# Kernel tuning notes

Measured on AMD Instinct MI355X. Metric: run time of the kernel, lower is better.

Reference implementation:

```python
import jax, jax.numpy as jnp
import numpy as np

N_NODES = 4096
N_EDGES = 8192
N_GRAPHS = 256
D_NODE = 64
D_EDGE = 32
H = 256


def setup_inputs() -> dict:
    key = jax.random.key(0)
    ks = jax.random.split(key, 16)
    s = lambda d: 1.0 / np.sqrt(d)
    inp = {
        "x": jax.random.normal(ks[0], (N_NODES, D_NODE), dtype=jnp.float32),
        "edge_index": jax.random.randint(ks[1], (2, N_EDGES), 0, N_NODES),
        "edge_attr": jax.random.normal(ks[2], (N_EDGES, D_EDGE), dtype=jnp.float32),
        "batch": jnp.sort(jax.random.randint(ks[3], (N_NODES,), 0, N_GRAPHS)),
        # conv1: edge MLP 32 -> 64*256, root weight 64->256, bias 256
        "nn1_w": jax.random.normal(ks[4], (D_EDGE, D_NODE * H), dtype=jnp.float32) * s(D_EDGE),
        "nn1_b": jnp.zeros((D_NODE * H,), dtype=jnp.float32),
        "root1_w": jax.random.normal(ks[5], (D_NODE, H), dtype=jnp.float32) * s(D_NODE),
        "bias1": jnp.zeros((H,), dtype=jnp.float32),
        # conv2: edge MLP 32 -> 256*256, root weight 256->256, bias 256
        "nn2_w": jax.random.normal(ks[6], (D_EDGE, H * H), dtype=jnp.float32) * s(D_EDGE),
        "nn2_b": jnp.zeros((H * H,), dtype=jnp.float32),
        "root2_w": jax.random.normal(ks[7], (H, H), dtype=jnp.float32) * s(H),
        "bias2": jnp.zeros((H,), dtype=jnp.float32),
        # readout MLP: 256 -> 128 -> 1
        "lin1_w": jax.random.normal(ks[8], (H, H // 2), dtype=jnp.float32) * s(H),
        "lin1_b": jnp.zeros((H // 2,), dtype=jnp.float32),
        "lin2_w": jax.random.normal(ks[9], (H // 2, 1), dtype=jnp.float32) * s(H // 2),
        "lin2_b": jnp.zeros((1,), dtype=jnp.float32),
    }
    return inp


def nnconv(x, src, dst, edge_attr, nn_w, nn_b, root_w, bias, out_c):
    # PyG NNConv (aggr='add'): per-edge weight matrix from edge MLP,
    # message = x[src] @ W_e, scatter-add at dst, plus root transform + bias.
    e = edge_attr.shape[0]
    in_c = x.shape[1]
    w_e = (edge_attr @ nn_w + nn_b).reshape(e, in_c, out_c)  # [E, in, out]
    msg = jnp.einsum('ei,eio->eo', x[src], w_e)              # [E, out]
    agg = jax.ops.segment_sum(msg, dst, num_segments=x.shape[0])
    return agg + x @ root_w + bias


def reference(x, edge_index, edge_attr, batch,
              nn1_w, nn1_b, root1_w, bias1,
              nn2_w, nn2_b, root2_w, bias2,
              lin1_w, lin1_b, lin2_w, lin2_b):
    src, dst = edge_index[0], edge_index[1]
    h = nnconv(x, src, dst, edge_attr, nn1_w, nn1_b, root1_w, bias1, H)
    h = jax.nn.relu(h)
    h = nnconv(h, src, dst, edge_attr, nn2_w, nn2_b, root2_w, bias2, H)
    # global mean pool over graphs
    sums = jax.ops.segment_sum(h, batch, num_segments=N_GRAPHS)
    cnts = jax.ops.segment_sum(jnp.ones((h.shape[0],), h.dtype), batch, num_segments=N_GRAPHS)
    pooled = sums / jnp.maximum(cnts, 1.0)[:, None]
    # dropout is identity in eval mode
    z = jax.nn.relu(pooled @ lin1_w + lin1_b)
    return jax.nn.sigmoid(z @ lin2_w + lin2_b)  # [N_GRAPHS, 1]
```

## Files before the change

### kernel.cpp

```cpp
#include <hip/hip_runtime.h>
#include <math.h>

#define N_NODES 4096
#define N_EDGES 8192
#define N_GRAPHS 256
#define D_NODE 64
#define D_EDGE 32
#define HH 256

#define K1 2176
#define K2 8704

typedef _Float16 half8v __attribute__((ext_vector_type(8)));
typedef _Float16 half4v __attribute__((ext_vector_type(4)));
typedef float floatx4 __attribute__((ext_vector_type(4)));

static const size_t OFF_S    = 0;
static const size_t OFF_BT1  = 17825792;
static const size_t OFF_BT2  = 18104320;
static const size_t OFF_CP   = 19218432;
static const size_t OFF_H    = 31801344;
static const size_t OFF_H2   = 32063488;
static const size_t OFF_INT  = 33112064;

__global__ __launch_bounds__(1024) void csr_k(const int* __restrict__ dst,
                                              int* __restrict__ starts,
                                              int* __restrict__ elist) {
    __shared__ int cnt[4096];
    __shared__ int part[1024];
    int t = threadIdx.x;
#pragma unroll
    for (int i = 0; i < 4; ++i) cnt[t * 4 + i] = 0;
    __syncthreads();
#pragma unroll
    for (int i = 0; i < 8; ++i) atomicAdd(&cnt[dst[i * 1024 + t]], 1);
    __syncthreads();
    int v[4]; int s = 0;
#pragma unroll
    for (int i = 0; i < 4; ++i) { v[i] = cnt[t * 4 + i]; s += v[i]; }
    part[t] = s;
    __syncthreads();
    for (int off = 1; off < 1024; off <<= 1) {
        int tv = (t >= off) ? part[t - off] : 0;
        __syncthreads();
        part[t] += tv;
        __syncthreads();
    }
    int excl = part[t] - s;
    __syncthreads();
#pragma unroll
    for (int i = 0; i < 4; ++i) {
        starts[t * 4 + i] = excl;
        cnt[t * 4 + i] = excl;
        excl += v[i];
    }
    if (t == 1023) starts[4096] = excl;
    __syncthreads();
#pragma unroll
    for (int i = 0; i < 8; ++i) {
        int e = i * 1024 + t;
        int d = dst[e];
        int p = atomicAdd(&cnt[d], 1);
        elist[p] = e;
    }
}

__device__ __forceinline__ void packT_body(const float* __restrict__ w,
                                           const float* __restrict__ b,
                                           const float* __restrict__ rw,
                                           _Float16* __restrict__ BT,
                                           int kk0, int o0, int K,
                                           int wlim, int blim, int wshift, int wmask, int wrow) {
    __shared__ float T[64][65];
    int t = threadIdx.x;
    int ol = t & 63, kb = t >> 6;
#pragma unroll
    for (int p = 0; p < 16; ++p) {
        int kl = p * 4 + kb;
        int kk = kk0 + kl, o = o0 + ol;
        float v;
        if (kk < wlim)      v = w[(kk >> wshift) * wrow + (kk & wmask) * 256 + o];
        else if (kk < blim) v = b[(kk - wlim) * 256 + o];
        else                v = rw[(kk - blim) * 256 + o];
        T[kl][ol] = v;
    }
    __syncthreads();
    int kl2 = t & 63, ob = t >> 6;
#pragma unroll
    for (int p = 0; p < 16; ++p) {
        int ol2 = p * 4 + ob;
        BT[(size_t)(o0 + ol2) * K + kk0 + kl2] = (_Float16)T[kl2][ol2];
    }
}

__global__ __launch_bounds__(256) void pack_k(const float* __restrict__ w1,
                                              const float* __restrict__ b1,
                                              const float* __restrict__ r1,
                                              const float* __restrict__ w2,
                                              const float* __restrict__ b2,
                                              const float* __restrict__ r2,
                                              _Float16* __restrict__ BT1,
                                              _Float16* __restrict__ BT2) {
    int bx = blockIdx.x, o0 = blockIdx.y * 64;
    if (bx < K1 / 64)
        packT_body(w1, b1, r1, BT1, bx * 64, o0, K1, 2048, 2112, 6, 63, 16384);
    else
        packT_body(w2, b2, r2, BT2, (bx - K1 / 64) * 64, o0, K2, 8192, 8448, 8, 255, 65536);
}

__global__ __launch_bounds__(64) void s1_k(const float* __restrict__ x,
                                           const float* __restrict__ ea,
                                           const int* __restrict__ src,
                                           const int* __restrict__ starts,
                                           const int* __restrict__ elist,
                                           _Float16* __restrict__ S) {
    int n = blockIdx.x, t = threadIdx.x;
    __shared__ float sea[33];
    if (t == 32) sea[32] = 1.0f;
    float acc[33];
#pragma unroll
    for (int k = 0; k < 33; ++k) acc[k] = 0.f;
    int st = starts[n], en = starts[n + 1];
    for (int idx = st; idx < en; ++idx) {
        int e = elist[idx];
        int sn = src[e];
        if (t < 32) sea[t] = ea[e * 32 + t];
        __syncthreads();
        float xv = x[sn * 64 + t];
#pragma unroll
        for (int k = 0; k < 33; ++k) acc[k] += sea[k] * xv;
        __syncthreads();
    }
    _Float16* row = S + (size_t)n * K1;
#pragma unroll
    for (int k = 0; k < 33; ++k) row[k * 64 + t] = (_Float16)acc[k];
    row[2112 + t] = (_Float16)x[n * 64 + t];
}

__global__ __launch_bounds__(256) void s2_k(const _Float16* __restrict__ h,
                                            const float* __restrict__ ea,
                                            const int* __restrict__ src,
                                            const int* __restrict__ starts,
                                            const int* __restrict__ elist,
                                            _Float16* __restrict__ S) {
    int n = blockIdx.x, t = threadIdx.x;
    __shared__ float sea[33];
    if (t == 32) sea[32] = 1.0f;
    float acc[33];
#pragma unroll
    for (int k = 0; k < 33; ++k) acc[k] = 0.f;
    int st = starts[n], en = starts[n + 1];
    for (int idx = st; idx < en; ++idx) {
        int e = elist[idx];
        int sn = src[e];
        if (t < 32) sea[t] = ea[e * 32 + t];
        __syncthreads();
        float hv = (float)h[sn * 256 + t];
#pragma unroll
        for (int k = 0; k < 33; ++k) acc[k] += sea[k] * hv;
        __syncthreads();
    }
    _Float16* row = S + (size_t)n * K2;
#pragma unroll
    for (int k = 0; k < 33; ++k) row[k * 256 + t] = (_Float16)acc[k];
    row[8448 + t] = h[n * 256 + t];
}

__device__ __forceinline__ void async_copy16(const void* g, void* l) {
    __builtin_amdgcn_global_load_lds(
        (__attribute__((address_space(1))) unsigned int*)(g),
        (__attribute__((address_space(3))) unsigned int*)(l), 16, 0, 0);
}

__global__ __launch_bounds__(256, 3) void gemm_f16(const _Float16* __restrict__ A,
                                                   const _Float16* __restrict__ BT,
                                                   float* __restrict__ Cpart,
                                                   int K, int NC, int Z) {
    __shared__ _Float16 As[128 * 64];
    __shared__ _Float16 Bs[128 * 64];
    int tid = threadIdx.x;
    int w = tid >> 6, l = tid & 63;
    int mt = blockIdx.y, nt = blockIdx.x, z = blockIdx.z;
    int c0 = z * NC / Z, c1 = (z + 1) * NC / Z;
    int k0 = c0 * 64;
    int wm = w & 1, wn = w >> 1;

    int lr = l >> 3, lc = l & 7;
    int gc = lc ^ lr;
    const _Float16* gA0 = A  + (size_t)(mt * 128 + w * 32 + lr) * K + k0 + gc * 8;
    const _Float16* gB0 = BT + (size_t)(nt * 128 + w * 32 + lr) * K + k0 + gc * 8;

    int lm = l & 15, q4 = l >> 4;
    int sw = lm & 7;

    floatx4 acc[4][4] = {};

    for (int s = c0; s < c1; ++s) {
#pragma unroll
        for (int q = 0; q < 4; ++q) {
            async_copy16(gA0 + (size_t)q * 8 * K, As + (w * 32 + q * 8) * 64);
            async_copy16(gB0 + (size_t)q * 8 * K, Bs + (w * 32 + q * 8) * 64);
        }
        gA0 += 64; gB0 += 64;
        __syncthreads();
#pragma unroll
        for (int kw = 0; kw < 2; ++kw) {
            int ck = ((kw * 4 + q4) ^ sw) * 8;
            half8v af[4], bf[4];
#pragma unroll
            for (int i = 0; i < 4; ++i)
                af[i] = *(const half8v*)&As[(wm * 64 + i * 16 + lm) * 64 + ck];
#pragma unroll
            for (int j = 0; j < 4; ++j)
                bf[j] = *(const half8v*)&Bs[(wn * 64 + j * 16 + lm) * 64 + ck];
#pragma unroll
            for (int i = 0; i < 4; ++i)
#pragma unroll
                for (int j = 0; j < 4; ++j)
                    acc[i][j] = __builtin_amdgcn_mfma_f32_16x16x32_f16(af[i], bf[j], acc[i][j], 0, 0, 0);
        }
        __syncthreads();
    }

    float* Cp = Cpart + (size_t)z * (N_NODES * HH);
    int m0 = mt * 128 + wm * 64;
    int n0 = nt * 128 + wn * 64 + lm;
#pragma unroll
    for (int i = 0; i < 4; ++i)
#pragma unroll
        for (int j = 0; j < 4; ++j)
#pragma unroll
            for (int r = 0; r < 4; ++r)
                Cp[(size_t)(m0 + i * 16 + q4 * 4 + r) * HH + n0 + j * 16] = acc[i][j][r];
}

__global__ __launch_bounds__(256) void reduce_k(const float* __restrict__ Cp,
                                                const float* __restrict__ bias,
                                                _Float16* __restrict__ o16,
                                                float* __restrict__ o32,
                                                int nslices, int relu) {
    int idx = (blockIdx.x * 256 + threadIdx.x) * 4;
    float4 a = *(const float4*)(Cp + idx);
    for (int zz = 1; zz < nslices; ++zz) {
        float4 bq = *(const float4*)(Cp + (size_t)zz * (N_NODES * HH) + idx);
        a.x += bq.x; a.y += bq.y; a.z += bq.z; a.w += bq.w;
    }
    int n = idx & 255;
    float4 bb = *(const float4*)(bias + n);
    a.x += bb.x; a.y += bb.y; a.z += bb.z; a.w += bb.w;
    if (relu) {
        a.x = fmaxf(a.x, 0.f); a.y = fmaxf(a.y, 0.f);
        a.z = fmaxf(a.z, 0.f); a.w = fmaxf(a.w, 0.f);
    }
    if (o16) {
        half4v hv = {(_Float16)a.x, (_Float16)a.y, (_Float16)a.z, (_Float16)a.w};
        *(half4v*)(o16 + idx) = hv;
    } else {
        *(float4*)(o32 + idx) = a;
    }
}

__global__ __launch_bounds__(128) void poolread_k(const float* __restrict__ h2,
                                                  const int* __restrict__ batch,
                                                  const float* __restrict__ l1w,
                                                  const float* __restrict__ l1b,
                                                  const float* __restrict__ l2w,
                                                  const float* __restrict__ l2b,
                                                  float* __restrict__ out) {
    int g = blockIdx.x, t = threadIdx.x;
    __shared__ int bnds[2];
    __shared__ float sp[256];
    __shared__ float sz[128];
    if (t < 2) {
        int target = g + t;
        int lo = 0, hi = N_NODES;
        while (lo < hi) { int mid = (lo + hi) >> 1; if (batch[mid] < target) lo = mid + 1; else hi = mid; }
        bnds[t] = lo;
    }
    __syncthreads();
    int lo = bnds[0], hi = bnds[1];
    float s0 = 0.f, s1 = 0.f;
    for (int n = lo; n < hi; ++n) {
        s0 += h2[(size_t)n * 256 + t];
        s1 += h2[(size_t)n * 256 + 128 + t];
    }
    float inv = 1.0f / fmaxf((float)(hi - lo), 1.0f);
    sp[t] = s0 * inv;
    sp[t + 128] = s1 * inv;
    __syncthreads();
    float a = l1b[t];
#pragma unroll 8
    for (int i = 0; i < 256; ++i) a += sp[i] * l1w[i * 128 + t];
    sz[t] = fmaxf(a, 0.f) * l2w[t];
    __syncthreads();
    for (int s = 64; s > 0; s >>= 1) {
        if (t < s) sz[t] += sz[t + s];
        __syncthreads();
    }
    if (t == 0) {
        float zz = sz[0] + l2b[0];
        out[g] = 1.0f / (1.0f + expf(-zz));
    }
}

extern "C" void kernel_launch(void* const* d_in, const int* in_sizes, int n_in,
                              void* d_out, int out_size, void* d_ws, size_t ws_size,
                              hipStream_t stream) {
    const float* x       = (const float*)d_in[0];
    const int*   ei      = (const int*)d_in[1];
    const float* ea      = (const float*)d_in[2];
    const int*   batch   = (const int*)d_in[3];
    const float* nn1_w   = (const float*)d_in[4];
    const float* nn1_b   = (const float*)d_in[5];
    const float* root1_w = (const float*)d_in[6];
    const float* bias1   = (const float*)d_in[7];
    const float* nn2_w   = (const float*)d_in[8];
    const float* nn2_b   = (const float*)d_in[9];
    const float* root2_w = (const float*)d_in[10];
    const float* bias2   = (const float*)d_in[11];
    const float* lin1_w  = (const float*)d_in[12];
    const float* lin1_b  = (const float*)d_in[13];
    const float* lin2_w  = (const float*)d_in[14];
    const float* lin2_b  = (const float*)d_in[15];
    float* out = (float*)d_out;
    float* ws  = (float*)d_ws;

    _Float16* S    = (_Float16*)(ws + OFF_S);
    _Float16* BT1  = (_Float16*)(ws + OFF_BT1);
    _Float16* BT2  = (_Float16*)(ws + OFF_BT2);
    float*    Cp   = ws + OFF_CP;
    _Float16* h    = (_Float16*)(ws + OFF_H);
    float*    h2   = ws + OFF_H2;
    int* ip     = (int*)(ws + OFF_INT);
    int* starts = ip;
    int* elist  = ip + 4100;

    const int* srcv = ei;
    const int* dstv = ei + N_EDGES;

    csr_k<<<1, 1024, 0, stream>>>(dstv, starts, elist);
    pack_k<<<dim3(K1 / 64 + K2 / 64, 4), 256, 0, stream>>>(nn1_w, nn1_b, root1_w,
                                                           nn2_w, nn2_b, root2_w, BT1, BT2);

    s1_k<<<4096, 64, 0, stream>>>(x, ea, srcv, starts, elist, S);
    gemm_f16<<<dim3(2, 32, 8), 256, 0, stream>>>(S, BT1, Cp, K1, K1 / 64, 8);
    reduce_k<<<1024, 256, 0, stream>>>(Cp, bias1, h, nullptr, 8, 1);

    s2_k<<<4096, 256, 0, stream>>>(h, ea, srcv, starts, elist, S);
    gemm_f16<<<dim3(2, 32, 12), 256, 0, stream>>>(S, BT2, Cp, K2, K2 / 64, 12);
    reduce_k<<<1024, 256, 0, stream>>>(Cp, bias2, nullptr, h2, 12, 0);

    poolread_k<<<N_GRAPHS, 128, 0, stream>>>(h2, batch, lin1_w, lin1_b, lin2_w, lin2_b, out);
}
```

Measured before the change: 206.9 us.

## Fuse edge-gather into GEMM A-tile load and fold reduce into pooling

Drops the separate s1/s2 kernels that built the large fp16 S matrix. Each GEMM block now builds its A tile on the fly: it gathers source-node features weighted by edge attributes for its rows and writes the swizzled tile into LDS, so S never goes through global memory. CSR construction is merged into the weight-packing launch, and the conv2 split-K reduction plus bias is folded into the pooling kernel, which cuts two launches and the h2 buffer. In exchange the gather is repeated per N-tile, its loads are irregular and sit inside the GEMM loop, and reduce_k gains a stray null-pointer dereference expression that is undefined behaviour.

Result: slower. 274.0 us (+32.4%).

```diff
diff --git a/kernel.cpp b/kernel.cpp
--- a/kernel.cpp
+++ b/kernel.cpp
@@ -10,67 +10,65 @@
 
 #define K1 2176
 #define K2 8704
+#define NSL1 8
+#define NSL2 12
 
 typedef _Float16 half8v __attribute__((ext_vector_type(8)));
-typedef _Float16 half4v __attribute__((ext_vector_type(4)));
 typedef float floatx4 __attribute__((ext_vector_type(4)));
 
-static const size_t OFF_S    = 0;
-static const size_t OFF_BT1  = 17825792;
-static const size_t OFF_BT2  = 18104320;
-static const size_t OFF_CP   = 19218432;
-static const size_t OFF_H    = 31801344;
-static const size_t OFF_H2   = 32063488;
-static const size_t OFF_INT  = 33112064;
-
-__global__ __launch_bounds__(1024) void csr_k(const int* __restrict__ dst,
-                                              int* __restrict__ starts,
-                                              int* __restrict__ elist) {
+static const size_t OFF_CP   = 0;
+static const size_t OFF_BT1  = 12582912;
+static const size_t OFF_BT2  = 12861440;
+static const size_t OFF_H    = 13975552;
+static const size_t OFF_INT  = 14499840;
+
+__device__ void csr_body(const int* __restrict__ dst,
+                         int* __restrict__ starts,
+                         int* __restrict__ elist) {
     __shared__ int cnt[4096];
-    __shared__ int part[1024];
+    __shared__ int ps[256];
     int t = threadIdx.x;
 #pragma unroll
-    for (int i = 0; i < 4; ++i) cnt[t * 4 + i] = 0;
-    __syncthreads();
-#pragma unroll
-    for (int i = 0; i < 8; ++i) atomicAdd(&cnt[dst[i * 1024 + t]], 1);
-    __syncthreads();
-    int v[4]; int s = 0;
-#pragma unroll
-    for (int i = 0; i < 4; ++i) { v[i] = cnt[t * 4 + i]; s += v[i]; }
-    part[t] = s;
-    __syncthreads();
-    for (int off = 1; off < 1024; off <<= 1) {
-        int tv = (t >= off) ? part[t - off] : 0;
-        __syncthreads();
-        part[t] += tv;
-        __syncthreads();
-    }
-    int excl = part[t] - s;
-    __syncthreads();
-#pragma unroll
-    for (int i = 0; i < 4; ++i) {
-        starts[t * 4 + i] = excl;
-        cnt[t * 4 + i] = excl;
+    for (int i = 0; i < 16; ++i) cnt[t * 16 + i] = 0;
+    __syncthreads();
+#pragma unroll
+    for (int i = 0; i < 32; ++i) atomicAdd(&cnt[dst[i * 256 + t]], 1);
+    __syncthreads();
+    int v[16]; int s = 0;
+#pragma unroll
+    for (int i = 0; i < 16; ++i) { v[i] = cnt[t * 16 + i]; s += v[i]; }
+    ps[t] = s;
+    __syncthreads();
+    for (int off = 1; off < 256; off <<= 1) {
+        int tv = (t >= off) ? ps[t - off] : 0;
+        __syncthreads();
+        ps[t] += tv;
+        __syncthreads();
+    }
+    int excl = ps[t] - s;
+#pragma unroll
+    for (int i = 0; i < 16; ++i) {
+        starts[t * 16 + i] = excl;
+        cnt[t * 16 + i] = excl;
         excl += v[i];
     }
-    if (t == 1023) starts[4096] = excl;
-    __syncthreads();
-#pragma unroll
-    for (int i = 0; i < 8; ++i) {
-        int e = i * 1024 + t;
+    if (t == 255) starts[4096] = excl;
+    __syncthreads();
+#pragma unroll
+    for (int i = 0; i < 32; ++i) {
+        int e = i * 256 + t;
         int d = dst[e];
         int p = atomicAdd(&cnt[d], 1);
         elist[p] = e;
     }
 }
 
-__device__ __forceinline__ void packT_body(const float* __restrict__ w,
-                                           const float* __restrict__ b,
-                                           const float* __restrict__ rw,
-                                           _Float16* __restrict__ BT,
-                                           int kk0, int o0, int K,
-                                           int wlim, int blim, int wshift, int wmask, int wrow) {
+__device__ void packT_body(const float* __restrict__ w,
+                           const float* __restrict__ b,
+                           const float* __restrict__ rw,
+                           _Float16* __restrict__ BT,
+                           int kk0, int o0, int K,
+                           int wlim, int blim, int wshift, int wmask, int wrow) {
     __shared__ float T[64][65];
     int t = threadIdx.x;
     int ol = t & 63, kb = t >> 6;
@@ -93,7 +91,10 @@
     }
 }
 
-__global__ __launch_bounds__(256) void pack_k(const float* __restrict__ w1,
+__global__ __launch_bounds__(256) void prep_k(const int* __restrict__ dst,
+                                              int* __restrict__ starts,
+                                              int* __restrict__ elist,
+                                              const float* __restrict__ w1,
                                               const float* __restrict__ b1,
                                               const float* __restrict__ r1,
                                               const float* __restrict__ w2,
@@ -101,69 +102,16 @@
                                               const float* __restrict__ r2,
                                               _Float16* __restrict__ BT1,
                                               _Float16* __restrict__ BT2) {
-    int bx = blockIdx.x, o0 = blockIdx.y * 64;
-    if (bx < K1 / 64)
-        packT_body(w1, b1, r1, BT1, bx * 64, o0, K1, 2048, 2112, 6, 63, 16384);
+    int bx = blockIdx.x, by = blockIdx.y;
+    if (bx == 0) {
+        if (by == 0) csr_body(dst, starts, elist);
+        return;
+    }
+    int pbx = bx - 1, o0 = by * 64;
+    if (pbx < K1 / 64)
+        packT_body(w1, b1, r1, BT1, pbx * 64, o0, K1, 2048, 2112, 6, 63, 16384);
     else
-        packT_body(w2, b2, r2, BT2, (bx - K1 / 64) * 64, o0, K2, 8192, 8448, 8, 255, 65536);
-}
-
-__global__ __launch_bounds__(64) void s1_k(const float* __restrict__ x,
-                                           const float* __restrict__ ea,
-                                           const int* __restrict__ src,
-                                           const int* __restrict__ starts,
-                                           const int* __restrict__ elist,
-                                           _Float16* __restrict__ S) {
-    int n = blockIdx.x, t = threadIdx.x;
-    __shared__ float sea[33];
-    if (t == 32) sea[32] = 1.0f;
-    float acc[33];
-#pragma unroll
-    for (int k = 0; k < 33; ++k) acc[k] = 0.f;
-    int st = starts[n], en = starts[n + 1];
-    for (int idx = st; idx < en; ++idx) {
-        int e = elist[idx];
-        int sn = src[e];
-        if (t < 32) sea[t] = ea[e * 32 + t];
-        __syncthreads();
-        float xv = x[sn * 64 + t];
-#pragma unroll
-        for (int k = 0; k < 33; ++k) acc[k] += sea[k] * xv;
-        __syncthreads();
-    }
-    _Float16* row = S + (size_t)n * K1;
-#pragma unroll
-    for (int k = 0; k < 33; ++k) row[k * 64 + t] = (_Float16)acc[k];
-    row[2112 + t] = (_Float16)x[n * 64 + t];
-}
-
-__global__ __launch_bounds__(256) void s2_k(const _Float16* __restrict__ h,
-                                            const float* __restrict__ ea,
-                                            const int* __restrict__ src,
-                                            const int* __restrict__ starts,
-                                            const int* __restrict__ elist,
-                                            _Float16* __restrict__ S) {
-    int n = blockIdx.x, t = threadIdx.x;
-    __shared__ float sea[33];
-    if (t == 32) sea[32] = 1.0f;
-    float acc[33];
-#pragma unroll
-    for (int k = 0; k < 33; ++k) acc[k] = 0.f;
-    int st = starts[n], en = starts[n + 1];
-    for (int idx = st; idx < en; ++idx) {
-        int e = elist[idx];
-        int sn = src[e];
-        if (t < 32) sea[t] = ea[e * 32 + t];
-        __syncthreads();
-        float hv = (float)h[sn * 256 + t];
-#pragma unroll
-        for (int k = 0; k < 33; ++k) acc[k] += sea[k] * hv;
-        __syncthreads();
-    }
-    _Float16* row = S + (size_t)n * K2;
-#pragma unroll
-    for (int k = 0; k < 33; ++k) row[k * 256 + t] = (_Float16)acc[k];
-    row[8448 + t] = h[n * 256 + t];
+        packT_body(w2, b2, r2, BT2, (pbx - K1 / 64) * 64, o0, K2, 8192, 8448, 8, 255, 65536);
 }
 
 __device__ __forceinline__ void async_copy16(const void* g, void* l) {
@@ -172,36 +120,84 @@
         (__attribute__((address_space(3))) unsigned int*)(l), 16, 0, 0);
 }
 
-__global__ __launch_bounds__(256, 3) void gemm_f16(const _Float16* __restrict__ A,
-                                                   const _Float16* __restrict__ BT,
-                                                   float* __restrict__ Cpart,
-                                                   int K, int NC, int Z) {
+template <typename T, int CPK>
+__global__ __launch_bounds__(256, 3) void gemm_fused(const T* __restrict__ X,
+                                                     const float* __restrict__ ea,
+                                                     const int* __restrict__ src,
+                                                     const int* __restrict__ starts,
+                                                     const int* __restrict__ elist,
+                                                     const _Float16* __restrict__ BT,
+                                                     float* __restrict__ Cpart,
+                                                     int K, int NC, int Z) {
     __shared__ _Float16 As[128 * 64];
     __shared__ _Float16 Bs[128 * 64];
+    const int ID = 64 * CPK;
     int tid = threadIdx.x;
     int w = tid >> 6, l = tid & 63;
-    int mt = blockIdx.y, nt = blockIdx.x, z = blockIdx.z;
+    int nt = blockIdx.x, mt = blockIdx.y, z = blockIdx.z;
     int c0 = z * NC / Z, c1 = (z + 1) * NC / Z;
-    int k0 = c0 * 64;
     int wm = w & 1, wn = w >> 1;
 
     int lr = l >> 3, lc = l & 7;
     int gc = lc ^ lr;
-    const _Float16* gA0 = A  + (size_t)(mt * 128 + w * 32 + lr) * K + k0 + gc * 8;
-    const _Float16* gB0 = BT + (size_t)(nt * 128 + w * 32 + lr) * K + k0 + gc * 8;
-
-    int lm = l & 15, q4 = l >> 4;
-    int sw = lm & 7;
+    const _Float16* gB0 = BT + (size_t)(nt * 128 + w * 32 + lr) * K + c0 * 64 + gc * 8;
+
+    int gr = tid >> 1, hs = tid & 1;
+    int n = mt * 128 + gr;
+    int e0 = starts[n], e1 = starts[n + 1];
+
+    int lm = l & 15, q4 = l >> 4, sw = lm & 7;
 
     floatx4 acc[4][4] = {};
 
-    for (int s = c0; s < c1; ++s) {
-#pragma unroll
-        for (int q = 0; q < 4; ++q) {
-            async_copy16(gA0 + (size_t)q * 8 * K, As + (w * 32 + q * 8) * 64);
+    for (int c = c0; c < c1; ++c) {
+#pragma unroll
+        for (int q = 0; q < 4; ++q)
             async_copy16(gB0 + (size_t)q * 8 * K, Bs + (w * 32 + q * 8) * 64);
+        gB0 += 64;
+
+        float ga[32];
+        int k = c / CPK;
+        if (k < 33) {
+            int i0 = (c - k * CPK) * 64 + hs * 32;
+#pragma unroll
+            for (int j = 0; j < 32; ++j) ga[j] = 0.f;
+            for (int ie = e0; ie < e1; ++ie) {
+                int e = elist[ie];
+                float val = (k == 32) ? 1.0f : ea[e * 32 + k];
+                const T* xp = X + (size_t)src[e] * ID + i0;
+                if (sizeof(T) == 2) {
+                    const half8v* hp = (const half8v*)xp;
+#pragma unroll
+                    for (int q = 0; q < 4; ++q) {
+                        half8v hv = hp[q];
+#pragma unroll
+                        for (int j = 0; j < 8; ++j) ga[q * 8 + j] += val * (float)hv[j];
+                    }
+                } else {
+                    const float4* fp = (const float4*)xp;
+#pragma unroll
+                    for (int q = 0; q < 8; ++q) {
+                        float4 fv = fp[q];
+                        ga[q * 4 + 0] += val * fv.x; ga[q * 4 + 1] += val * fv.y;
+                        ga[q * 4 + 2] += val * fv.z; ga[q * 4 + 3] += val * fv.w;
+                    }
+                }
+            }
+        } else {
+            const T* xp = X + (size_t)n * ID + (c - 33 * CPK) * 64 + hs * 32;
+#pragma unroll
+            for (int j = 0; j < 32; ++j) ga[j] = (float)xp[j];
         }
-        gA0 += 64; gB0 += 64;
+        _Float16* arow = As + gr * 64;
+#pragma unroll
+        for (int c8 = 0; c8 < 4; ++c8) {
+            int slot = (hs * 4 + c8) ^ (gr & 7);
+            half8v hv;
+#pragma unroll
+            for (int j = 0; j < 8; ++j) hv[j] = (_Float16)ga[c8 * 8 + j];
+            *(half8v*)(arow + slot * 8) = hv;
+        }
         __syncthreads();
 #pragma unroll
         for (int kw = 0; kw < 2; ++kw) {
@@ -236,32 +232,26 @@
 
 __global__ __launch_bounds__(256) void reduce_k(const float* __restrict__ Cp,
                                                 const float* __restrict__ bias,
-                                                _Float16* __restrict__ o16,
-                                                float* __restrict__ o32,
-                                                int nslices, int relu) {
+                                                _Float16* __restrict__ o16) {
     int idx = (blockIdx.x * 256 + threadIdx.x) * 4;
     float4 a = *(const float4*)(Cp + idx);
-    for (int zz = 1; zz < nslices; ++zz) {
+#pragma unroll
+    for (int zz = 1; zz < NSL1; ++zz) {
         float4 bq = *(const float4*)(Cp + (size_t)zz * (N_NODES * HH) + idx);
         a.x += bq.x; a.y += bq.y; a.z += bq.z; a.w += bq.w;
     }
-    int n = idx & 255;
-    float4 bb = *(const float4*)(bias + n);
-    a.x += bb.x; a.y += bb.y; a.z += bb.z; a.w += bb.w;
-    if (relu) {
-        a.x = fmaxf(a.x, 0.f); a.y = fmaxf(a.y, 0.f);
-        a.z = fmaxf(a.z, 0.f); a.w = fmaxf(a.w, 0.f);
-    }
-    if (o16) {
-        half4v hv = {(_Float16)a.x, (_Float16)a.y, (_Float16)a.z, (_Float16)a.w};
-        *(half4v*)(o16 + idx) = hv;
-    } else {
-        *(float4*)(o32 + idx) = a;
-    }
-}
-
-__global__ __launch_bounds__(128) void poolread_k(const float* __restrict__ h2,
+    int nn = idx & 255;
+    float4 bb = *(const float4*)(bias + nn);
+    a.x = fmaxf(a.x + bb.x, 0.f); a.y = fmaxf(a.y + bb.y, 0.f);
+    a.z = fmaxf(a.z + bb.z, 0.f); a.w = fmaxf(a.w + bb.w, 0.f);
+    _Float16 h4[4] = {(_Float16)a.x, (_Float16)a.y, (_Float16)a.z, (_Float16)a.w};
+    *(half8v*)0;
+    o16[idx + 0] = h4[0]; o16[idx + 1] = h4[1]; o16[idx + 2] = h4[2]; o16[idx + 3] = h4[3];
+}
+
+__global__ __launch_bounds__(256) void poolread_k(const float* __restrict__ Cp,
                                                   const int* __restrict__ batch,
+                                                  const float* __restrict__ bias2,
                                                   const float* __restrict__ l1w,
                                                   const float* __restrict__ l1b,
                                                   const float* __restrict__ l2w,
@@ -279,22 +269,27 @@
     }
     __syncthreads();
     int lo = bnds[0], hi = bnds[1];
-    float s0 = 0.f, s1 = 0.f;
+    float s = 0.f;
     for (int n = lo; n < hi; ++n) {
-        s0 += h2[(size_t)n * 256 + t];
-        s1 += h2[(size_t)n * 256 + 128 + t];
-    }
-    float inv = 1.0f / fmaxf((float)(hi - lo), 1.0f);
-    sp[t] = s0 * inv;
-    sp[t + 128] = s1 * inv;
-    __syncthreads();
-    float a = l1b[t];
+        float a = 0.f;
+#pragma unroll
+        for (int zz = 0; zz < NSL2; ++zz)
+            a += Cp[(size_t)zz * (N_NODES * HH) + (size_t)n * HH + t];
+        s += a;
+    }
+    sp[t] = (hi > lo) ? (s / (float)(hi - lo) + bias2[t]) : 0.f;
+    __syncthreads();
+    float r = 0.f;
+    if (t < 128) {
+        float a = l1b[t];
 #pragma unroll 8
-    for (int i = 0; i < 256; ++i) a += sp[i] * l1w[i * 128 + t];
-    sz[t] = fmaxf(a, 0.f) * l2w[t];
-    __syncthreads();
-    for (int s = 64; s > 0; s >>= 1) {
-        if (t < s) sz[t] += sz[t + s];
+        for (int i = 0; i < 256; ++i) a += sp[i] * l1w[i * 128 + t];
+        r = fmaxf(a, 0.f) * l2w[t];
+        sz[t] = r;
+    }
+    __syncthreads();
+    for (int ss = 64; ss > 0; ss >>= 1) {
+        if (t < ss) sz[t] += sz[t + ss];
         __syncthreads();
     }
     if (t == 0) {
@@ -325,12 +320,10 @@
     float* out = (float*)d_out;
     float* ws  = (float*)d_ws;
 
-    _Float16* S    = (_Float16*)(ws + OFF_S);
-    _Float16* BT1  = (_Float16*)(ws + OFF_BT1);
-    _Float16* BT2  = (_Float16*)(ws + OFF_BT2);
-    float*    Cp   = ws + OFF_CP;
-    _Float16* h    = (_Float16*)(ws + OFF_H);
-    float*    h2   = ws + OFF_H2;
+    float*    Cp  = ws + OFF_CP;
+    _Float16* BT1 = (_Float16*)(ws + OFF_BT1);
+    _Float16* BT2 = (_Float16*)(ws + OFF_BT2);
+    _Float16* h   = (_Float16*)(ws + OFF_H);
     int* ip     = (int*)(ws + OFF_INT);
     int* starts = ip;
     int* elist  = ip + 4100;
@@ -338,17 +331,17 @@
     const int* srcv = ei;
     const int* dstv = ei + N_EDGES;
 
-    csr_k<<<1, 1024, 0, stream>>>(dstv, starts, elist);
-    pack_k<<<dim3(K1 / 64 + K2 / 64, 4), 256, 0, stream>>>(nn1_w, nn1_b, root1_w,
-                                                           nn2_w, nn2_b, root2_w, BT1, BT2);
-
-    s1_k<<<4096, 64, 0, stream>>>(x, ea, srcv, starts, elist, S);
-    gemm_f16<<<dim3(2, 32, 8), 256, 0, stream>>>(S, BT1, Cp, K1, K1 / 64, 8);
-    reduce_k<<<1024, 256, 0, stream>>>(Cp, bias1, h, nullptr, 8, 1);
-
-    s2_k<<<4096, 256, 0, stream>>>(h, ea, srcv, starts, elist, S);
-    gemm_f16<<<dim3(2, 32, 12), 256, 0, stream>>>(S, BT2, Cp, K2, K2 / 64, 12);
-    reduce_k<<<1024, 256, 0, stream>>>(Cp, bias2, nullptr, h2, 12, 0);
-
-    poolread_k<<<N_GRAPHS, 128, 0, stream>>>(h2, batch, lin1_w, lin1_b, lin2_w, lin2_b, out);
-}
+    prep_k<<<dim3(1 + K1 / 64 + K2 / 64, 4), 256, 0, stream>>>(
+        dstv, starts, elist, nn1_w, nn1_b, root1_w, nn2_w, nn2_b, root2_w, BT1, BT2);
+
+    gemm_fused<float, 1><<<dim3(2, 32, NSL1), 256, 0, stream>>>(
+        x, ea, srcv, starts, elist, BT1, Cp, K1, K1 / 64, NSL1);
+
+    reduce_k<<<1024, 256, 0, stream>>>(Cp, bias1, h);
+
+    gemm_fused<_Float16, 4><<<dim3(2, 32, NSL2), 256, 0, stream>>>(
+        h, ea, srcv, starts, elist, BT2, Cp, K2, K2 / 64, NSL2);
+
+    poolread_k<<<N_GRAPHS, 256, 0, stream>>>(Cp, batch, bias2,
+                                             lin1_w, lin1_b, lin2_w, lin2_b, out);
+}
```

## Store split-K partials in fp16 and fuse reductions into consumers

Applied to the files above, without the earlier changes.

GEMM split-K partial outputs are now written as fp16 instead of fp32, which halves partial-sum traffic. The second-layer reduce kernel is removed, and the mean-pool readout now sums the slice partials per node directly and adds bias2 after averaging. The CSR build is merged into the weight-pack kernel as an extra block, and the first reduce becomes a vectorised 8-wide fp16 kernel. This drops two launches and much memory traffic, at the cost of fp16 rounding on partial sums, which may lose accuracy, and a longer serial loop in poolread.

After: 200.5 us. 3.1% less time.

```diff
diff --git a/kernel.cpp b/kernel.cpp
--- a/kernel.cpp
+++ b/kernel.cpp
@@ -10,67 +10,66 @@
 
 #define K1 2176
 #define K2 8704
+#define NSL1 8
+#define NSL2 12
 
 typedef _Float16 half8v __attribute__((ext_vector_type(8)));
-typedef _Float16 half4v __attribute__((ext_vector_type(4)));
 typedef float floatx4 __attribute__((ext_vector_type(4)));
 
 static const size_t OFF_S    = 0;
 static const size_t OFF_BT1  = 17825792;
 static const size_t OFF_BT2  = 18104320;
 static const size_t OFF_CP   = 19218432;
-static const size_t OFF_H    = 31801344;
-static const size_t OFF_H2   = 32063488;
-static const size_t OFF_INT  = 33112064;
-
-__global__ __launch_bounds__(1024) void csr_k(const int* __restrict__ dst,
-                                              int* __restrict__ starts,
-                                              int* __restrict__ elist) {
+static const size_t OFF_H    = 25509888;
+static const size_t OFF_INT  = 26034176;
+
+__device__ void csr_body(const int* __restrict__ dst,
+                         int* __restrict__ starts,
+                         int* __restrict__ elist) {
     __shared__ int cnt[4096];
-    __shared__ int part[1024];
+    __shared__ int ps[256];
     int t = threadIdx.x;
 #pragma unroll
-    for (int i = 0; i < 4; ++i) cnt[t * 4 + i] = 0;
-    __syncthreads();
-#pragma unroll
-    for (int i = 0; i < 8; ++i) atomicAdd(&cnt[dst[i * 1024 + t]], 1);
-    __syncthreads();
-    int v[4]; int s = 0;
-#pragma unroll
-    for (int i = 0; i < 4; ++i) { v[i] = cnt[t * 4 + i]; s += v[i]; }
-    part[t] = s;
-    __syncthreads();
-    for (int off = 1; off < 1024; off <<= 1) {
-        int tv = (t >= off) ? part[t - off] : 0;
-        __syncthreads();
-        part[t] += tv;
-        __syncthreads();
-    }
-    int excl = part[t] - s;
-    __syncthreads();
-#pragma unroll
-    for (int i = 0; i < 4; ++i) {
-        starts[t * 4 + i] = excl;
-        cnt[t * 4 + i] = excl;
+    for (int i = 0; i < 16; ++i) cnt[t * 16 + i] = 0;
+    __syncthreads();
+#pragma unroll
+    for (int i = 0; i < 32; ++i) atomicAdd(&cnt[dst[i * 256 + t]], 1);
+    __syncthreads();
+    int v[16]; int s = 0;
+#pragma unroll
+    for (int i = 0; i < 16; ++i) { v[i] = cnt[t * 16 + i]; s += v[i]; }
+    ps[t] = s;
+    __syncthreads();
+    for (int off = 1; off < 256; off <<= 1) {
+        int tv = (t >= off) ? ps[t - off] : 0;
+        __syncthreads();
+        ps[t] += tv;
+        __syncthreads();
+    }
+    int excl = ps[t] - s;
+#pragma unroll
+    for (int i = 0; i < 16; ++i) {
+        starts[t * 16 + i] = excl;
+        cnt[t * 16 + i] = excl;
         excl += v[i];
     }
-    if (t == 1023) starts[4096] = excl;
-    __syncthreads();
-#pragma unroll
-    for (int i = 0; i < 8; ++i) {
-        int e = i * 1024 + t;
+    if (t == 255) starts[4096] = excl;
+    __syncthreads();
+#pragma unroll
+    for (int i = 0; i < 32; ++i) {
+        int e = i * 256 + t;
         int d = dst[e];
         int p = atomicAdd(&cnt[d], 1);
         elist[p] = e;
     }
 }
 
-__device__ __forceinline__ void packT_body(const float* __restrict__ w,
-                                           const float* __restrict__ b,
-                                           const float* __restrict__ rw,
-                                           _Float16* __restrict__ BT,
-                                           int kk0, int o0, int K,
-                                           int wlim, int blim, int wshift, int wmask, int wrow) {
+__device__ void packT_body(const float* __restrict__ w,
+                           const float* __restrict__ b,
+                           const float* __restrict__ rw,
+                           _Float16* __restrict__ BT,
+                           int kk0, int o0, int K,
+                           int wlim, int blim, int wshift, int wmask, int wrow) {
     __shared__ float T[64][65];
     int t = threadIdx.x;
     int ol = t & 63, kb = t >> 6;
@@ -93,7 +92,10 @@
     }
 }
 
-__global__ __launch_bounds__(256) void pack_k(const float* __restrict__ w1,
+__global__ __launch_bounds__(256) void prep_k(const int* __restrict__ dst,
+                                              int* __restrict__ starts,
+                                              int* __restrict__ elist,
+                                              const float* __restrict__ w1,
                                               const float* __restrict__ b1,
                                               const float* __restrict__ r1,
                                               const float* __restrict__ w2,
@@ -101,11 +103,16 @@
                                               const float* __restrict__ r2,
                                               _Float16* __restrict__ BT1,
                                               _Float16* __restrict__ BT2) {
-    int bx = blockIdx.x, o0 = blockIdx.y * 64;
-    if (bx < K1 / 64)
-        packT_body(w1, b1, r1, BT1, bx * 64, o0, K1, 2048, 2112, 6, 63, 16384);
+    int bx = blockIdx.x, by = blockIdx.y;
+    if (bx == 0) {
+        if (by == 0) csr_body(dst, starts, elist);
+        return;
+    }
+    int pbx = bx - 1, o0 = by * 64;
+    if (pbx < K1 / 64)
+        packT_body(w1, b1, r1, BT1, pbx * 64, o0, K1, 2048, 2112, 6, 63, 16384);
     else
-        packT_body(w2, b2, r2, BT2, (bx - K1 / 64) * 64, o0, K2, 8192, 8448, 8, 255, 65536);
+        packT_body(w2, b2, r2, BT2, (pbx - K1 / 64) * 64, o0, K2, 8192, 8448, 8, 255, 65536);
 }
 
 __global__ __launch_bounds__(64) void s1_k(const float* __restrict__ x,
@@ -174,7 +181,7 @@
 
 __global__ __launch_bounds__(256, 3) void gemm_f16(const _Float16* __restrict__ A,
                                                    const _Float16* __restrict__ BT,
-                                                   float* __restrict__ Cpart,
+                                                   _Float16* __restrict__ Cpart,
                                                    int K, int NC, int Z) {
     __shared__ _Float16 As[128 * 64];
     __shared__ _Float16 Bs[128 * 64];
@@ -222,7 +229,7 @@
         __syncthreads();
     }
 
-    float* Cp = Cpart + (size_t)z * (N_NODES * HH);
+    _Float16* Cp = Cpart + (size_t)z * (N_NODES * HH);
     int m0 = mt * 128 + wm * 64;
     int n0 = nt * 128 + wn * 64 + lm;
 #pragma unroll
@@ -231,37 +238,30 @@
         for (int j = 0; j < 4; ++j)
 #pragma unroll
             for (int r = 0; r < 4; ++r)
-                Cp[(size_t)(m0 + i * 16 + q4 * 4 + r) * HH + n0 + j * 16] = acc[i][j][r];
-}
-
-__global__ __launch_bounds__(256) void reduce_k(const float* __restrict__ Cp,
-                                                const float* __restrict__ bias,
-                                                _Float16* __restrict__ o16,
-                                                float* __restrict__ o32,
-                                                int nslices, int relu) {
-    int idx = (blockIdx.x * 256 + threadIdx.x) * 4;
-    float4 a = *(const float4*)(Cp + idx);
-    for (int zz = 1; zz < nslices; ++zz) {
-        float4 bq = *(const float4*)(Cp + (size_t)zz * (N_NODES * HH) + idx);
-        a.x += bq.x; a.y += bq.y; a.z += bq.z; a.w += bq.w;
-    }
-    int n = idx & 255;
-    float4 bb = *(const float4*)(bias + n);
-    a.x += bb.x; a.y += bb.y; a.z += bb.z; a.w += bb.w;
-    if (relu) {
-        a.x = fmaxf(a.x, 0.f); a.y = fmaxf(a.y, 0.f);
-        a.z = fmaxf(a.z, 0.f); a.w = fmaxf(a.w, 0.f);
-    }
-    if (o16) {
-        half4v hv = {(_Float16)a.x, (_Float16)a.y, (_Float16)a.z, (_Float16)a.w};
-        *(half4v*)(o16 + idx) = hv;
-    } else {
-        *(float4*)(o32 + idx) = a;
-    }
-}
-
-__global__ __launch_bounds__(128) void poolread_k(const float* __restrict__ h2,
+                Cp[(size_t)(m0 + i * 16 + q4 * 4 + r) * HH + n0 + j * 16] = (_Float16)acc[i][j][r];
+}
+
+__global__ __launch_bounds__(256) void hep_k(const _Float16* __restrict__ Cp,
+                                             const float* __restrict__ bias,
+                                             _Float16* __restrict__ h) {
+    int idx = (blockIdx.x * 256 + threadIdx.x) * 8;
+    float a[8] = {};
+#pragma unroll
+    for (int zz = 0; zz < NSL1; ++zz) {
+        half8v v = *(const half8v*)(Cp + (size_t)zz * (N_NODES * HH) + idx);
+#pragma unroll
+        for (int j = 0; j < 8; ++j) a[j] += (float)v[j];
+    }
+    int col = idx & 255;
+    half8v o;
+#pragma unroll
+    for (int j = 0; j < 8; ++j) o[j] = (_Float16)fmaxf(a[j] + bias[col + j], 0.f);
+    *(half8v*)(h + idx) = o;
+}
+
+__global__ __launch_bounds__(256) void poolread_k(const _Float16* __restrict__ Cp,
                                                   const int* __restrict__ batch,
+                                                  const float* __restrict__ bias2,
                                                   const float* __restrict__ l1w,
                                                   const float* __restrict__ l1b,
                                                   const float* __restrict__ l2w,
@@ -279,22 +279,23 @@
     }
     __syncthreads();
     int lo = bnds[0], hi = bnds[1];
-    float s0 = 0.f, s1 = 0.f;
+    float s = 0.f;
     for (int n = lo; n < hi; ++n) {
-        s0 += h2[(size_t)n * 256 + t];
-        s1 += h2[(size_t)n * 256 + 128 + t];
-    }
-    float inv = 1.0f / fmaxf((float)(hi - lo), 1.0f);
-    sp[t] = s0 * inv;
-    sp[t + 128] = s1 * inv;
-    __syncthreads();
-    float a = l1b[t];
+#pragma unroll
+        for (int zz = 0; zz < NSL2; ++zz)
+            s += (float)Cp[(size_t)zz * (N_NODES * HH) + (size_t)n * HH + t];
+    }
+    sp[t] = (hi > lo) ? (s / (float)(hi - lo) + bias2[t]) : 0.f;
+    __syncthreads();
+    if (t < 128) {
+        float a = l1b[t];
 #pragma unroll 8
-    for (int i = 0; i < 256; ++i) a += sp[i] * l1w[i * 128 + t];
-    sz[t] = fmaxf(a, 0.f) * l2w[t];
-    __syncthreads();
-    for (int s = 64; s > 0; s >>= 1) {
-        if (t < s) sz[t] += sz[t + s];
+        for (int i = 0; i < 256; ++i) a += sp[i] * l1w[i * 128 + t];
+        sz[t] = fmaxf(a, 0.f) * l2w[t];
+    }
+    __syncthreads();
+    for (int ss = 64; ss > 0; ss >>= 1) {
+        if (t < ss) sz[t] += sz[t + ss];
         __syncthreads();
     }
     if (t == 0) {
@@ -325,12 +326,11 @@
     float* out = (float*)d_out;
     float* ws  = (float*)d_ws;
 
-    _Float16* S    = (_Float16*)(ws + OFF_S);
-    _Float16* BT1  = (_Float16*)(ws + OFF_BT1);
-    _Float16* BT2  = (_Float16*)(ws + OFF_BT2);
-    float*    Cp   = ws + OFF_CP;
-    _Float16* h    = (_Float16*)(ws + OFF_H);
-    float*    h2   = ws + OFF_H2;
+    _Float16* S   = (_Float16*)(ws + OFF_S);
+    _Float16* BT1 = (_Float16*)(ws + OFF_BT1);
+    _Float16* BT2 = (_Float16*)(ws + OFF_BT2);
+    _Float16* Cp  = (_Float16*)(ws + OFF_CP);
+    _Float16* h   = (_Float16*)(ws + OFF_H);
     int* ip     = (int*)(ws + OFF_INT);
     int* starts = ip;
     int* elist  = ip + 4100;
@@ -338,17 +338,19 @@
     const int* srcv = ei;
     const int* dstv = ei + N_EDGES;
 
-    csr_k<<<1, 1024, 0, stream>>>(dstv, starts, elist);
-    pack_k<<<dim3(K1 / 64 + K2 / 64, 4), 256, 0, stream>>>(nn1_w, nn1_b, root1_w,
-                                                           nn2_w, nn2_b, root2_w, BT1, BT2);
+    prep_k<<<dim3(1 + K1 / 64 + K2 / 64, 4), 256, 0, stream>>>(
+        dstv, starts, elist, nn1_w, nn1_b, root1_w, nn2_w, nn2_b, root2_w, BT1, BT2);
 
     s1_k<<<4096, 64, 0, stream>>>(x, ea, srcv, starts, elist, S);
-    gemm_f16<<<dim3(2, 32, 8), 256, 0, stream>>>(S, BT1, Cp, K1, K1 / 64, 8);
-    reduce_k<<<1024, 256, 0, stream>>>(Cp, bias1, h, nullptr, 8, 1);
+
+    gemm_f16<<<dim3(2, 32, NSL1), 256, 0, stream>>>(S, BT1, Cp, K1, K1 / 64, NSL1);
+
+    hep_k<<<512, 256, 0, stream>>>(Cp, bias1, h);
 
     s2_k<<<4096, 256, 0, stream>>>(h, ea, srcv, starts, elist, S);
-    gemm_f16<<<dim3(2, 32, 12), 256, 0, stream>>>(S, BT2, Cp, K2, K2 / 64, 12);
-    reduce_k<<<1024, 256, 0, stream>>>(Cp, bias2, nullptr, h2, 12, 0);
-
-    poolread_k<<<N_GRAPHS, 128, 0, stream>>>(h2, batch, lin1_w, lin1_b, lin2_w, lin2_b, out);
-}
+
+    gemm_f16<<<dim3(2, 32, NSL2), 256, 0, stream>>>(S, BT2, Cp, K2, K2 / 64, NSL2);
+
+    poolread_k<<<N_GRAPHS, 256, 0, stream>>>(Cp, batch, bias2,
+                                             lin1_w, lin1_b, lin2_w, lin2_b, out);
+}
```
